# Optimization experiments

Measured on AMD Instinct MI355X. Metric: run time of the kernel, lower is better.

## Reference

```python
import jax, jax.numpy as jnp
import numpy as np

B, L, D, H = 2, 512, 1024, 16
DH = D // H  # head_dim = 64


def setup_inputs() -> dict:
    key = jax.random.key(0)
    ks = jax.random.split(key, 14)
    s = 0.02
    inp = {
        "x": jax.random.normal(ks[0], (B, L, D), jnp.float32),
        "q1_w": jax.random.normal(ks[1], (D, D), jnp.float32) * s,
        "q1_b": jax.random.normal(ks[2], (D,), jnp.float32) * s,
        "k1_w": jax.random.normal(ks[3], (D, D), jnp.float32) * s,
        "k1_b": jax.random.normal(ks[4], (D,), jnp.float32) * s,
        "k2_w": jax.random.normal(ks[5], (D, D), jnp.float32) * s,
        "k2_b": jax.random.normal(ks[6], (D,), jnp.float32) * s,
        "gw_w": jax.random.normal(ks[7], (DH, 1), jnp.float32) * s,
        "gw_b": jax.random.normal(ks[8], (1,), jnp.float32) * s,
        "sw_w": jax.random.normal(ks[9], (DH, 1), jnp.float32) * s,
        "sw_b": jax.random.normal(ks[10], (1,), jnp.float32) * s,
        "cp_w": jax.random.normal(ks[11], (D, D), jnp.float32) * s,
        "cp_b": jax.random.normal(ks[12], (D,), jnp.float32) * s,
    }
    return inp


def reference(x, q1_w, q1_b, k1_w, k1_b, k2_w, k2_b, gw_w, gw_b, sw_w, sw_b, cp_w, cp_b):
    b, l, dm = x.shape
    dh = gw_w.shape[0]
    h = dm // dh
    Q = (x @ q1_w + q1_b).reshape(b, l, h, dh)              # (B,L,H,d)
    K = (x @ k1_w + k1_b).reshape(b, l, h, dh)              # (B,L,H,d)
    V = x.reshape(b, l, h, dh)                               # (B,L,H,d)
    # outer-product state K ⊗ V : (B,L,H,d,d)
    W = K[..., :, None] * V[..., None, :]
    # gate -> stable cumulative product along L (log-space, clamped)
    G = jax.nn.sigmoid(x.reshape(b, l, h, dh) @ gw_w + gw_b)          # (B,L,H,1)
    log_cp = jnp.clip(jnp.cumsum(jnp.log(jnp.clip(G, 1e-6, None)), axis=1), -30.0, 30.0)
    Gc = (jnp.exp(log_cp) + 1e-6)[..., None]                 # (B,L,H,1,1)
    # decay branch
    R = jax.nn.silu(K @ sw_w + sw_b)[..., None]              # (B,L,H,1,1)
    # weighted (invertible) cumsum: cumsum(x / cumprod) * cumprod
    Wc = jnp.cumsum(W * R / Gc, axis=1) * Gc                 # (B,L,H,d,d)
    O1 = jnp.einsum('blhd,blhde->blhe', Q, Wc)               # (B,L,H,d)
    # MA branch on residuals
    E = V[:, 1:] - O1[:, :-1]                                # (B,L-1,H,d)
    sd = jnp.sqrt(jnp.asarray(dh, x.dtype))
    q2 = -jax.nn.leaky_relu(-Q[:, :-1] / sd, 0.02)           # ma_q_activation
    sD = jnp.sqrt(jnp.asarray(dm, x.dtype))
    k2 = jax.nn.sigmoid((x[:, :-1] @ k2_w + k2_b) / sD * 0.02).reshape(b, l - 1, h, dh)
    Wma = jnp.cumsum(k2[..., :, None] * E[..., None, :], axis=1)  # (B,L-1,H,d,d)
    O2 = jnp.einsum('blhd,blhde->blhe', q2, Wma)             # (B,L-1,H,d)
    O2 = jnp.concatenate([jnp.zeros_like(O2[:, :1]), O2], axis=1)  # (B,L,H,d)
    y = (O1 + O2).reshape(b, l, dm)
    return y @ cp_w + cp_b
```

## Files before the change

### kernel.cpp

```cpp
#include <hip/hip_runtime.h>
#include <hip/hip_bf16.h>
#include <math.h>


typedef unsigned short ushort_t;
typedef __attribute__((ext_vector_type(8))) short bf16x8;
typedef __attribute__((ext_vector_type(4))) float f32x4;

__device__ __forceinline__ float sigmoidf_(float z) { return 1.f / (1.f + expf(-z)); }

__device__ __forceinline__ ushort_t f2bf(float f) {
    __hip_bfloat16 h = __float2bfloat16(f);
    return *reinterpret_cast<ushort_t*>(&h);
}

__device__ __forceinline__ float bf2f(ushort_t u) {
    union { unsigned int i; float f; } v;
    v.i = ((unsigned int)u) << 16;
    return v.f;
}

__device__ __forceinline__ void gl16(const void* g, void* l) {
    __builtin_amdgcn_global_load_lds(
        (const __attribute__((address_space(1))) unsigned int*)g,
        (__attribute__((address_space(3))) unsigned int*)l, 16, 0, 0);
}

__global__ __launch_bounds__(256) void cvtT(const float* __restrict__ xs,
                                            const float* __restrict__ w0, const float* __restrict__ w1,
                                            const float* __restrict__ w2, const float* __restrict__ w3,
                                            ushort_t* __restrict__ xd,
                                            ushort_t* __restrict__ t0, ushort_t* __restrict__ t1,
                                            ushort_t* __restrict__ t2, ushort_t* __restrict__ t3) {
    const int blk = blockIdx.x;
    const int tid = threadIdx.x;
    if (blk >= 1024) {
        const int off = ((blk - 1024) * 256 + tid) * 8;
        float4 a = *reinterpret_cast<const float4*>(xs + off);
        float4 b = *reinterpret_cast<const float4*>(xs + off + 4);
        union { uint4 v; ushort_t u[8]; } pk;
        pk.u[0] = f2bf(a.x); pk.u[1] = f2bf(a.y); pk.u[2] = f2bf(a.z); pk.u[3] = f2bf(a.w);
        pk.u[4] = f2bf(b.x); pk.u[5] = f2bf(b.y); pk.u[6] = f2bf(b.z); pk.u[7] = f2bf(b.w);
        *reinterpret_cast<uint4*>(xd + off) = pk.v;
        return;
    }
    const int wi = blk >> 8;
    const float* W = wi == 0 ? w0 : wi == 1 ? w1 : wi == 2 ? w2 : w3;
    ushort_t* WT = wi == 0 ? t0 : wi == 1 ? t1 : wi == 2 ? t2 : t3;
    const int tile = blk & 255;
    const int k0 = (tile >> 4) * 64, n0 = (tile & 15) * 64;
    __shared__ ushort_t T[64][72];
#pragma unroll
    for (int it = 0; it < 4; ++it) {
        const int idx = tid + it * 256;
        const int r = idx >> 4;
        const int c4 = (idx & 15) * 4;
        float4 v = *reinterpret_cast<const float4*>(W + (size_t)(k0 + r) * 1024 + n0 + c4);
        T[r][c4 + 0] = f2bf(v.x); T[r][c4 + 1] = f2bf(v.y);
        T[r][c4 + 2] = f2bf(v.z); T[r][c4 + 3] = f2bf(v.w);
    }
    __syncthreads();
    const int n = tid >> 2;
    const int kq = (tid & 3) * 16;
    union { uint4 v[2]; ushort_t u[16]; } pk;
#pragma unroll
    for (int j = 0; j < 16; ++j) pk.u[j] = T[kq + j][n];
    *reinterpret_cast<uint4*>(WT + (size_t)(n0 + n) * 1024 + k0 + kq) = pk.v[0];
    *reinterpret_cast<uint4*>(WT + (size_t)(n0 + n) * 1024 + k0 + kq + 8) = pk.v[1];
}

__global__ __launch_bounds__(256) void gemmQKC(const ushort_t* __restrict__ Ab,
                                               const ushort_t* __restrict__ WqT,
                                               const ushort_t* __restrict__ WkT,
                                               const ushort_t* __restrict__ WcT,
                                               const float* __restrict__ bq_,
                                               const float* __restrict__ bk_,
                                               const float* __restrict__ bc_,
                                               const float* __restrict__ x,
                                               const float* __restrict__ gww,
                                               const float* __restrict__ gwb,
                                               const float* __restrict__ sww,
                                               const float* __restrict__ swb,
                                               ushort_t* __restrict__ qb,
                                               ushort_t* __restrict__ q2b,
                                               ushort_t* __restrict__ kb,
                                               ushort_t* __restrict__ k2q,
                                               float* __restrict__ gc_out,
                                               float* __restrict__ ab_out,
                                               float* __restrict__ dS0) {
    const int sel = blockIdx.z;
    const ushort_t* WT = sel == 0 ? WqT : sel == 1 ? WkT : WcT;
    const float* bias = sel == 0 ? bq_ : sel == 1 ? bk_ : bc_;
    const int m0 = blockIdx.y * 64, n0 = blockIdx.x * 64;

    __shared__ __align__(16) char smem[32768];

    const int tid = threadIdx.x;
    const int w = tid >> 6, lane = tid & 63;
    const int l15 = lane & 15, lq = lane >> 4;

    f32x4 acc[4];
#pragma unroll
    for (int i = 0; i < 4; ++i) acc[i] = (f32x4){0.f, 0.f, 0.f, 0.f};

    auto stage = [&](int buf, int k0) {
        char* As = smem + buf * 8192;
        char* Bs = smem + 16384 + buf * 8192;
#pragma unroll
        for (int is = 0; is < 2; ++is) {
            const int p = tid * 16 + is * 4096;
            const int row = p >> 7;
            const int scb = (p & 127) ^ ((row & 7) << 4);
            gl16((const char*)Ab + (((size_t)(m0 + row)) << 11) + (k0 << 1) + scb,
                 As + is * 4096 + w * 1024);
            gl16((const char*)WT + (((size_t)(n0 + row)) << 11) + (k0 << 1) + scb,
                 Bs + is * 4096 + w * 1024);
        }
    };

    stage(0, 0);
    __syncthreads();
    for (int k0 = 0; k0 < 1024; k0 += 64) {
        const int cur = (k0 >> 6) & 1;
        if (k0 < 960) stage(cur ^ 1, k0 + 64);
        const char* As = smem + cur * 8192;
        const char* Bs = smem + 16384 + cur * 8192;
#pragma unroll
        for (int kk = 0; kk < 64; kk += 32) {
            const int cb = (kk + 8 * lq) * 2;
            const int ra = 16 * w + l15;
            bf16x8 a = *reinterpret_cast<const bf16x8*>(As + ra * 128 + (cb ^ ((ra & 7) << 4)));
#pragma unroll
            for (int nt = 0; nt < 4; ++nt) {
                const int rb = 16 * nt + l15;
                bf16x8 b = *reinterpret_cast<const bf16x8*>(Bs + rb * 128 + (cb ^ ((rb & 7) << 4)));
                acc[nt] = __builtin_amdgcn_mfma_f32_16x16x32_bf16(a, b, acc[nt], 0, 0, 0);
            }
        }
        __syncthreads();
    }

#pragma unroll
    for (int nt = 0; nt < 4; ++nt) {
        const int col = n0 + 16 * nt + l15;
        const float bcol = bias[col];
#pragma unroll
        for (int r = 0; r < 4; ++r) {
            acc[nt][r] += bcol;
            const int row = m0 + 16 * w + 4 * lq + r;
            const size_t o = (size_t)row * 1024 + col;
            const float v = acc[nt][r];
            if (sel == 0) {
                qb[o] = f2bf(v);
                q2b[o] = f2bf((v < 0.f ? v : 0.02f * v) * 0.125f);
            } else if (sel == 1) {
                kb[o] = f2bf(v);
            } else {
                k2q[o] = f2bf(sigmoidf_(v * 6.25e-4f));
            }
        }
    }

    if (sel != 1) return;

    typedef ushort_t row72[72];
    row72* KT = (row72*)smem;
    row72* VT = (row72*)(smem + 9216);
    float* gwl  = (float*)(smem + 18432);
    float* ctot = (float*)(smem + 18688);
    float* abl  = (float*)(smem + 18720);
    float* dkl  = (float*)(smem + 18976);
    const int b = blockIdx.y >> 3, j = blockIdx.y & 7;
    const int h = blockIdx.x;
    const int bh = b * 16 + h;
    const size_t xbase = (size_t)(b * 512) * 1024 + h * 64;

    if (tid < 64) gwl[tid] = gww[tid];

    {
        const float s0 = sww[l15], s1 = sww[16 + l15], s2 = sww[32 + l15], s3 = sww[48 + l15];
#pragma unroll
        for (int r = 0; r < 4; ++r) {
            float p = acc[0][r] * s0 + acc[1][r] * s1 + acc[2][r] * s2 + acc[3][r] * s3;
            p += __shfl_xor(p, 1, 64);
            p += __shfl_xor(p, 2, 64);
            p += __shfl_xor(p, 4, 64);
            p += __shfl_xor(p, 8, 64);
            if (l15 == 0) dkl[16 * w + 4 * lq + r] = p;
        }
    }
    __syncthreads();

    const float gwbv = gwb[0], swbv = swb[0];
    float ps_own = 0.f;
    for (int i = 0; i * 256 < (j + 1) * 64; ++i) {
        const int t = i * 256 + tid;
        const int cseg = i * 4 + w;
        if (cseg <= j) {
            const float* xr = x + xbase + (size_t)t * 1024;
            float dg = 0.f;
#pragma unroll
            for (int d = 0; d < 64; d += 4) {
                float4 xv = *reinterpret_cast<const float4*>(xr + d);
                dg += xv.x * gwl[d] + xv.y * gwl[d + 1] + xv.z * gwl[d + 2] + xv.w * gwl[d + 3];
            }
            const float g = sigmoidf_(dg + gwbv);
            float ps = logf(fmaxf(g, 1e-6f));
#pragma unroll
            for (int off = 1; off < 64; off <<= 1) {
                float v = __shfl_up(ps, off, 64);
                if (lane >= off) ps += v;
            }
            if (lane == 63) ctot[cseg] = ps;
            if (cseg == j) ps_own = ps;
        }
    }
    __syncthreads();
    if (w == (j & 3)) {
        float coff = 0.f;
        for (int cc = 0; cc < j; ++cc) coff += ctot[cc];
        const float lsum = coff + ps_own;
        const float Gc = expf(fminf(fmaxf(lsum, -30.f), 30.f)) + 1e-6f;
        const float z = dkl[lane] + swbv;
        const float a = z * sigmoidf_(z) / Gc;
        abl[lane] = a;
        gc_out[bh * 512 + j * 64 + lane] = Gc;
        ab_out[bh * 512 + j * 64 + lane] = a;
    }
    __syncthreads();

#pragma unroll
    for (int nt = 0; nt < 4; ++nt)
#pragma unroll
        for (int r = 0; r < 4; ++r)
            KT[16 * nt + l15][16 * w + 4 * lq + r] = f2bf(acc[nt][r]);
#pragma unroll
    for (int it = 0; it < 4; ++it) {
        const int idx = tid + it * 256;
        const int rr = idx >> 4;
        const int c4 = (idx & 15) << 2;
        float4 xv = *reinterpret_cast<const float4*>(x + xbase + (size_t)(j * 64 + rr) * 1024 + c4);
        const float a = abl[rr];
        VT[c4 + 0][rr] = f2bf(a * xv.x); VT[c4 + 1][rr] = f2bf(a * xv.y);
        VT[c4 + 2][rr] = f2bf(a * xv.z); VT[c4 + 3][rr] = f2bf(a * xv.w);
    }
    __syncthreads();

    f32x4 st[4];
#pragma unroll
    for (int n = 0; n < 4; ++n) st[n] = (f32x4){0.f, 0.f, 0.f, 0.f};
#pragma unroll
    for (int kk = 0; kk < 64; kk += 32) {
        bf16x8 ak = *reinterpret_cast<const bf16x8*>(&KT[16 * w + l15][kk + 8 * lq]);
#pragma unroll
        for (int n = 0; n < 4; ++n) {
            bf16x8 vb = *reinterpret_cast<const bf16x8*>(&VT[16 * n + l15][kk + 8 * lq]);
            st[n] = __builtin_amdgcn_mfma_f32_16x16x32_bf16(ak, vb, st[n], 0, 0, 0);
        }
    }
    float* o = dS0 + (size_t)(bh * 8 + j) * 4096;
#pragma unroll
    for (int n = 0; n < 4; ++n)
#pragma unroll
        for (int r = 0; r < 4; ++r)
            o[(16 * w + 4 * lq + r) * 64 + 16 * n + l15] = st[n][r];
}

__global__ __launch_bounds__(512) void out0_ds1(const float* __restrict__ x,
                                                const ushort_t* __restrict__ Qb,
                                                const ushort_t* __restrict__ Kb,
                                                const ushort_t* __restrict__ K2b,
                                                const float* __restrict__ gc,
                                                const float* __restrict__ ab,
                                                const float* __restrict__ dS0,
                                                float* __restrict__ O1out,
                                                float* __restrict__ dS1,
                                                ushort_t* __restrict__ EbT) {
    const int rt = blockIdx.x, bh = blockIdx.y;
    const int b = bh >> 4, h = bh & 15;
    const int c0 = rt * 64;
    const int tid = threadIdx.x;
    const int w = tid >> 6, lane = tid & 63;
    const int l15 = lane & 15, lq = lane >> 4;
    const int tw = w >> 1, eh = w & 1;

    __shared__ __align__(16) char Qs[8192];
    __shared__ __align__(16) char Ks[8192];
    __shared__ ushort_t VT[64][72];
    __shared__ ushort_t K2T[64][72];
    __shared__ ushort_t ET[64][72];
    __shared__ ushort_t Ps[64][72];
    __shared__ ushort_t SBt[64][72];
    __shared__ float av[64], gcv[64];

    const size_t base = (size_t)(b * 512) * 1024 + h * 64;
    const size_t rowB = (size_t)(b * 512 + c0) * 2048 + h * 128;

    {
        const int p = tid * 16;
        const int row = p >> 7;
        const int scb = (p & 127) ^ ((row & 7) << 4);
        gl16((const char*)Qb + rowB + (size_t)row * 2048 + scb, Qs + w * 1024);
        gl16((const char*)Kb + rowB + (size_t)row * 2048 + scb, Ks + w * 1024);
    }
#pragma unroll
    for (int it = 0; it < 2; ++it) {
        const int idx = tid + it * 512;
        const int rr = idx >> 4;
        const int c4 = (idx & 15) << 2;
        const int tau = c0 + rr;
        float4 xv = *reinterpret_cast<const float4*>(x + base + (size_t)tau * 1024 + c4);
        VT[c4 + 0][rr] = f2bf(xv.x); VT[c4 + 1][rr] = f2bf(xv.y);
        VT[c4 + 2][rr] = f2bf(xv.z); VT[c4 + 3][rr] = f2bf(xv.w);
        ushort4 cv = *reinterpret_cast<const ushort4*>(K2b + base + (size_t)tau * 1024 + c4);
        K2T[c4 + 0][rr] = cv.x; K2T[c4 + 1][rr] = cv.y;
        K2T[c4 + 2][rr] = cv.z; K2T[c4 + 3][rr] = cv.w;
    }
    if (tid < 64) av[tid] = ab[bh * 512 + c0 + tid];
    else if (tid < 128) gcv[tid - 64] = gc[bh * 512 + c0 + tid - 64];

#pragma unroll
    for (int ii = 0; ii < 2; ++ii) {
        const int flat = tid * 8 + ii * 4;
        float4 s = {0.f, 0.f, 0.f, 0.f};
        for (int jj = 0; jj < rt; ++jj) {
            float4 v = *reinterpret_cast<const float4*>(dS0 + (size_t)(bh * 8 + jj) * 4096 + flat);
            s.x += v.x; s.y += v.y; s.z += v.z; s.w += v.w;
        }
        const int d = flat >> 6, e = flat & 63;
        SBt[e + 0][d] = f2bf(s.x); SBt[e + 1][d] = f2bf(s.y);
        SBt[e + 2][d] = f2bf(s.z); SBt[e + 3][d] = f2bf(s.w);
    }
    __syncthreads();

    const int ra = 16 * tw + l15;
    f32x4 sc[2];
    sc[0] = (f32x4){0.f, 0.f, 0.f, 0.f};
    sc[1] = (f32x4){0.f, 0.f, 0.f, 0.f};
#pragma unroll
    for (int kk = 0; kk < 64; kk += 32) {
        const int cb = (kk + 8 * lq) * 2;
        bf16x8 aq = *reinterpret_cast<const bf16x8*>(Qs + ra * 128 + (cb ^ ((ra & 7) << 4)));
#pragma unroll
        for (int i = 0; i < 2; ++i) {
            const int rb = 16 * (2 * eh + i) + l15;
            bf16x8 bb = *reinterpret_cast<const bf16x8*>(Ks + rb * 128 + (cb ^ ((rb & 7) << 4)));
            sc[i] = __builtin_amdgcn_mfma_f32_16x16x32_bf16(aq, bb, sc[i], 0, 0, 0);
        }
    }
#pragma unroll
    for (int i = 0; i < 2; ++i) {
        const int cl = 16 * (2 * eh + i) + l15;
#pragma unroll
        for (int r = 0; r < 4; ++r) {
            const int tl = 16 * tw + 4 * lq + r;
            Ps[tl][cl] = f2bf(cl <= tl ? sc[i][r] * av[cl] : 0.f);
        }
    }
    __syncthreads();

    f32x4 oc[2];
    oc[0] = (f32x4){0.f, 0.f, 0.f, 0.f};
    oc[1] = (f32x4){0.f, 0.f, 0.f, 0.f};
#pragma unroll
    for (int kk = 0; kk < 64; kk += 32) {
        const int cb = (kk + 8 * lq) * 2;
        bf16x8 aq = *reinterpret_cast<const bf16x8*>(Qs + ra * 128 + (cb ^ ((ra & 7) << 4)));
        bf16x8 ap = *reinterpret_cast<const bf16x8*>(&Ps[16 * tw + l15][kk + 8 * lq]);
#pragma unroll
        for (int i = 0; i < 2; ++i) {
            const int nb = 16 * (2 * eh + i) + l15;
            bf16x8 sb = *reinterpret_cast<const bf16x8*>(&SBt[nb][kk + 8 * lq]);
            oc[i] = __builtin_amdgcn_mfma_f32_16x16x32_bf16(aq, sb, oc[i], 0, 0, 0);
            bf16x8 vb = *reinterpret_cast<const bf16x8*>(&VT[nb][kk + 8 * lq]);
            oc[i] = __builtin_amdgcn_mfma_f32_16x16x32_bf16(ap, vb, oc[i], 0, 0, 0);
        }
    }

#pragma unroll
    for (int i = 0; i < 2; ++i) {
        const int e = 16 * (2 * eh + i) + l15;
#pragma unroll
        for (int r = 0; r < 4; ++r) {
            const int tl = 16 * tw + 4 * lq + r;
            const int tau = c0 + tl;
            const float val = gcv[tl] * oc[i][r];
            O1out[base + (size_t)tau * 1024 + e] = val;
            float ev = 0.f;
            if (tau <= 510) ev = x[base + (size_t)(tau + 1) * 1024 + e] - val;
            ET[e][tl] = f2bf(ev);
        }
    }
    __syncthreads();

    {
        const int e = tid >> 3;
        const int tq = (tid & 7) * 8;
        uint4 v0 = *reinterpret_cast<const uint4*>(&ET[e][tq]);
        *reinterpret_cast<uint4*>(EbT + (size_t)(bh * 64 + e) * 512 + c0 + tq) = v0;
    }

    f32x4 st[2];
    st[0] = (f32x4){0.f, 0.f, 0.f, 0.f};
    st[1] = (f32x4){0.f, 0.f, 0.f, 0.f};
#pragma unroll
    for (int kk = 0; kk < 64; kk += 32) {
        bf16x8 ak = *reinterpret_cast<const bf16x8*>(&K2T[16 * tw + l15][kk + 8 * lq]);
#pragma unroll
        for (int i = 0; i < 2; ++i) {
            bf16x8 eb = *reinterpret_cast<const bf16x8*>(&ET[16 * (2 * eh + i) + l15][kk + 8 * lq]);
            st[i] = __builtin_amdgcn_mfma_f32_16x16x32_bf16(ak, eb, st[i], 0, 0, 0);
        }
    }
    float* o = dS1 + (size_t)(bh * 8 + rt) * 4096;
#pragma unroll
    for (int i = 0; i < 2; ++i)
#pragma unroll
        for (int r = 0; r < 4; ++r)
            o[(16 * tw + 4 * lq + r) * 64 + 16 * (2 * eh + i) + l15] = st[i][r];
}

__global__ __launch_bounds__(512) void out1_k(const ushort_t* __restrict__ Q2b,
                                              const ushort_t* __restrict__ K2b,
                                              const ushort_t* __restrict__ EbT,
                                              const float* __restrict__ O1,
                                              const float* __restrict__ dS1,
                                              ushort_t* __restrict__ yout) {
    const int rt = blockIdx.x, bh = blockIdx.y;
    const int b = bh >> 4, h = bh & 15;
    const int c0 = rt * 64;
    const int tid = threadIdx.x;
    const int w = tid >> 6, lane = tid & 63;
    const int l15 = lane & 15, lq = lane >> 4;
    const int tw = w >> 1, eh = w & 1;

    __shared__ __align__(16) char Q2s[8192];
    __shared__ __align__(16) char K2s[8192];
    __shared__ __align__(16) char ETs[8192];
    __shared__ ushort_t Ps[64][72];
    __shared__ ushort_t SBt[64][72];

    const size_t base = (size_t)(b * 512) * 1024 + h * 64;
    const size_t rowB = (size_t)(b * 512 + c0) * 2048 + h * 128;

    {
        const int p = tid * 16;
        const int row = p >> 7;
        const int scb = (p & 127) ^ ((row & 7) << 4);
        gl16((const char*)Q2b + rowB + (size_t)row * 2048 + scb, Q2s + w * 1024);
        gl16((const char*)K2b + rowB + (size_t)row * 2048 + scb, K2s + w * 1024);
        gl16((const char*)EbT + (size_t)(bh * 64 + row) * 1024 + c0 * 2 + scb, ETs + w * 1024);
    }
#pragma unroll
    for (int ii = 0; ii < 2; ++ii) {
        const int flat = tid * 8 + ii * 4;
        float4 s = {0.f, 0.f, 0.f, 0.f};
        for (int jj = 0; jj < rt; ++jj) {
            float4 v = *reinterpret_cast<const float4*>(dS1 + (size_t)(bh * 8 + jj) * 4096 + flat);
            s.x += v.x; s.y += v.y; s.z += v.z; s.w += v.w;
        }
        const int d = flat >> 6, e = flat & 63;
        SBt[e + 0][d] = f2bf(s.x); SBt[e + 1][d] = f2bf(s.y);
        SBt[e + 2][d] = f2bf(s.z); SBt[e + 3][d] = f2bf(s.w);
    }
    __syncthreads();

    const int ra = 16 * tw + l15;
    f32x4 sc[2];
    sc[0] = (f32x4){0.f, 0.f, 0.f, 0.f};
    sc[1] = (f32x4){0.f, 0.f, 0.f, 0.f};
#pragma unroll
    for (int kk = 0; kk < 64; kk += 32) {
        const int cb = (kk + 8 * lq) * 2;
        bf16x8 aq = *reinterpret_cast<const bf16x8*>(Q2s + ra * 128 + (cb ^ ((ra & 7) << 4)));
#pragma unroll
        for (int i = 0; i < 2; ++i) {
            const int rb = 16 * (2 * eh + i) + l15;
            bf16x8 bb = *reinterpret_cast<const bf16x8*>(K2s + rb * 128 + (cb ^ ((rb & 7) << 4)));
            sc[i] = __builtin_amdgcn_mfma_f32_16x16x32_bf16(aq, bb, sc[i], 0, 0, 0);
        }
    }
#pragma unroll
    for (int i = 0; i < 2; ++i) {
        const int cl = 16 * (2 * eh + i) + l15;
#pragma unroll
        for (int r = 0; r < 4; ++r) {
            const int tl = 16 * tw + 4 * lq + r;
            Ps[tl][cl] = f2bf(cl <= tl ? sc[i][r] : 0.f);
        }
    }
    __syncthreads();

    f32x4 oc[2];
    oc[0] = (f32x4){0.f, 0.f, 0.f, 0.f};
    oc[1] = (f32x4){0.f, 0.f, 0.f, 0.f};
#pragma unroll
    for (int kk = 0; kk < 64; kk += 32) {
        const int cb = (kk + 8 * lq) * 2;
        bf16x8 aq = *reinterpret_cast<const bf16x8*>(Q2s + ra * 128 + (cb ^ ((ra & 7) << 4)));
        bf16x8 ap = *reinterpret_cast<const bf16x8*>(&Ps[16 * tw + l15][kk + 8 * lq]);
#pragma unroll
        for (int i = 0; i < 2; ++i) {
            const int rb = 16 * (2 * eh + i) + l15;
            bf16x8 sb = *reinterpret_cast<const bf16x8*>(&SBt[rb][kk + 8 * lq]);
            oc[i] = __builtin_amdgcn_mfma_f32_16x16x32_bf16(aq, sb, oc[i], 0, 0, 0);
            bf16x8 eb = *reinterpret_cast<const bf16x8*>(ETs + rb * 128 + (cb ^ ((rb & 7) << 4)));
            oc[i] = __builtin_amdgcn_mfma_f32_16x16x32_bf16(ap, eb, oc[i], 0, 0, 0);
        }
    }

#pragma unroll
    for (int i = 0; i < 2; ++i) {
        const int e = 16 * (2 * eh + i) + l15;
#pragma unroll
        for (int r = 0; r < 4; ++r) {
            const int tp = c0 + 16 * tw + 4 * lq + r;
            if (tp <= 510) {
                yout[(size_t)(b * 512 + tp + 1) * 1024 + h * 64 + e] =
                    f2bf(O1[base + (size_t)(tp + 1) * 1024 + e] + oc[i][r]);
            }
        }
    }
    if (rt == 0 && tid < 64)
        yout[(size_t)(b * 512) * 1024 + h * 64 + tid] = f2bf(O1[base + tid]);
}

__global__ __launch_bounds__(512) void gemmP(const ushort_t* __restrict__ Ab,
                                             const ushort_t* __restrict__ WT,
                                             const float* __restrict__ bias,
                                             float* __restrict__ Out) {
    const int m0 = blockIdx.y * 64, n0 = blockIdx.x * 64;
    __shared__ __align__(16) char smem[32768];

    const int tid = threadIdx.x;
    const int w = tid >> 6, lane = tid & 63;
    const int l15 = lane & 15, lq = lane >> 4;
    const int mw = w >> 1, nh = w & 1;

    f32x4 acc[2];
    acc[0] = (f32x4){0.f, 0.f, 0.f, 0.f};
    acc[1] = (f32x4){0.f, 0.f, 0.f, 0.f};

    auto stage = [&](int buf, int k0) {
        const int p = tid * 16;
        const int row = p >> 7;
        const int scb = (p & 127) ^ ((row & 7) << 4);
        gl16((const char*)Ab + (((size_t)(m0 + row)) << 11) + (k0 << 1) + scb,
             smem + buf * 8192 + w * 1024);
        gl16((const char*)WT + (((size_t)(n0 + row)) << 11) + (k0 << 1) + scb,
             smem + 16384 + buf * 8192 + w * 1024);
    };

    stage(0, 0);
    __syncthreads();
    for (int k0 = 0; k0 < 1024; k0 += 64) {
        const int cur = (k0 >> 6) & 1;
        if (k0 < 960) stage(cur ^ 1, k0 + 64);
        const char* As = smem + cur * 8192;
        const char* Bs = smem + 16384 + cur * 8192;
#pragma unroll
        for (int kk = 0; kk < 64; kk += 32) {
            const int cb = (kk + 8 * lq) * 2;
            const int ra = 16 * mw + l15;
            bf16x8 a = *reinterpret_cast<const bf16x8*>(As + ra * 128 + (cb ^ ((ra & 7) << 4)));
#pragma unroll
            for (int i = 0; i < 2; ++i) {
                const int rb = 16 * (2 * nh + i) + l15;
                bf16x8 b = *reinterpret_cast<const bf16x8*>(Bs + rb * 128 + (cb ^ ((rb & 7) << 4)));
                acc[i] = __builtin_amdgcn_mfma_f32_16x16x32_bf16(a, b, acc[i], 0, 0, 0);
            }
        }
        __syncthreads();
    }
#pragma unroll
    for (int i = 0; i < 2; ++i) {
        const int col = n0 + 16 * (2 * nh + i) + l15;
        const float bcol = bias[col];
#pragma unroll
        for (int r = 0; r < 4; ++r) {
            const int row = m0 + 16 * mw + 4 * lq + r;
            Out[(size_t)row * 1024 + col] = acc[i][r] + bcol;
        }
    }
}

extern "C" void kernel_launch(void* const* d_in, const int* in_sizes, int n_in,
                              void* d_out, int out_size, void* d_ws, size_t ws_size,
                              hipStream_t stream) {
    const float* x   = (const float*)d_in[0];
    const float* q1w = (const float*)d_in[1];
    const float* q1b = (const float*)d_in[2];
    const float* k1w = (const float*)d_in[3];
    const float* k1b = (const float*)d_in[4];
    const float* k2w = (const float*)d_in[5];
    const float* k2b = (const float*)d_in[6];
    const float* gww = (const float*)d_in[7];
    const float* gwb = (const float*)d_in[8];
    const float* sww = (const float*)d_in[9];
    const float* swb = (const float*)d_in[10];
    const float* cpw = (const float*)d_in[11];
    const float* cpb = (const float*)d_in[12];
    float* out = (float*)d_out;

    float* ws = (float*)d_ws;
    float* O1   = ws;
    float* dS0b = ws + 1048576;
    float* dS1b = ws + 2097152;
    float* gcb  = ws + 3145728;
    float* abb  = ws + 3162112;
    ushort_t* ub = (ushort_t*)(ws + 3178496);
    ushort_t* xb   = ub;
    ushort_t* qb   = ub + 1048576;
    ushort_t* q2b  = ub + 2097152;
    ushort_t* kb   = ub + 3145728;
    ushort_t* k2q  = ub + 4194304;
    ushort_t* EbT  = ub + 5242880;
    ushort_t* wqT  = ub + 6291456;
    ushort_t* wkT  = ub + 7340032;
    ushort_t* wcT  = ub + 8388608;
    ushort_t* wpT  = ub + 9437184;
    ushort_t* ytb  = ub + 10485760;

    cvtT<<<1536, 256, 0, stream>>>(x, q1w, k1w, k2w, cpw, xb, wqT, wkT, wcT, wpT);
    gemmQKC<<<dim3(16, 16, 3), 256, 0, stream>>>(xb, wqT, wkT, wcT, q1b, k1b, k2b,
                                                 x, gww, gwb, sww, swb,
                                                 qb, q2b, kb, k2q, gcb, abb, dS0b);
    out0_ds1<<<dim3(8, 32), 512, 0, stream>>>(x, qb, kb, k2q, gcb, abb, dS0b, O1, dS1b, EbT);
    out1_k<<<dim3(8, 32), 512, 0, stream>>>(q2b, k2q, EbT, O1, dS1b, ytb);
    gemmP<<<dim3(16, 16), 512, 0, stream>>>(ytb, wpT, cpb, out);
}
```

Measured before the change: 60.86 us.

## Triple-buffer GEMM LDS staging with explicit vmcnt waits in projection kernels

Both bf16 MFMA GEMM kernels move from double to triple buffering of the A/B tiles in LDS. Loads are issued two iterations ahead, and the full __syncthreads is replaced by partial s_waitcnt vmcnt counts plus raw s_barrier, so global-to-LDS copies can overlap more compute. The loop is fully unrolled. LDS use per block grows from 32KB to 48KB, which may lower occupancy, and the hand-set vmcnt values must match the number of outstanding loads exactly.

Result: faster. 57.52 us (-5.5%).

```diff
diff --git a/kernel.cpp b/kernel.cpp
--- a/kernel.cpp
+++ b/kernel.cpp
@@ -93,7 +93,7 @@
     const float* bias = sel == 0 ? bq_ : sel == 1 ? bk_ : bc_;
     const int m0 = blockIdx.y * 64, n0 = blockIdx.x * 64;
 
-    __shared__ __align__(16) char smem[32768];
+    __shared__ __align__(16) char smem[49152];
 
     const int tid = threadIdx.x;
     const int w = tid >> 6, lane = tid & 63;
@@ -105,7 +105,7 @@
 
     auto stage = [&](int buf, int k0) {
         char* As = smem + buf * 8192;
-        char* Bs = smem + 16384 + buf * 8192;
+        char* Bs = smem + 24576 + buf * 8192;
 #pragma unroll
         for (int is = 0; is < 2; ++is) {
             const int p = tid * 16 + is * 4096;
@@ -119,12 +119,19 @@
     };
 
     stage(0, 0);
-    __syncthreads();
-    for (int k0 = 0; k0 < 1024; k0 += 64) {
-        const int cur = (k0 >> 6) & 1;
-        if (k0 < 960) stage(cur ^ 1, k0 + 64);
+    stage(1, 64);
+#pragma unroll
+    for (int it = 0; it < 16; ++it) {
+        const int k0 = it * 64;
+        const int cur = it % 3;
+        if (it < 14) stage((it + 2) % 3, k0 + 128);
+        if (it < 14)      asm volatile("s_waitcnt vmcnt(8)" ::: "memory");
+        else if (it == 14) asm volatile("s_waitcnt vmcnt(4)" ::: "memory");
+        else               asm volatile("s_waitcnt vmcnt(0)" ::: "memory");
+        __builtin_amdgcn_sched_barrier(0);
+        __builtin_amdgcn_s_barrier();
         const char* As = smem + cur * 8192;
-        const char* Bs = smem + 16384 + cur * 8192;
+        const char* Bs = smem + 24576 + cur * 8192;
 #pragma unroll
         for (int kk = 0; kk < 64; kk += 32) {
             const int cb = (kk + 8 * lq) * 2;
@@ -137,7 +144,9 @@
                 acc[nt] = __builtin_amdgcn_mfma_f32_16x16x32_bf16(a, b, acc[nt], 0, 0, 0);
             }
         }
-        __syncthreads();
+        asm volatile("s_waitcnt lgkmcnt(0)" ::: "memory");
+        __builtin_amdgcn_sched_barrier(0);
+        __builtin_amdgcn_s_barrier();
     }
 
 #pragma unroll
@@ -530,7 +539,7 @@
                                              const float* __restrict__ bias,
                                              float* __restrict__ Out) {
     const int m0 = blockIdx.y * 64, n0 = blockIdx.x * 64;
-    __shared__ __align__(16) char smem[32768];
+    __shared__ __align__(16) char smem[49152];
 
     const int tid = threadIdx.x;
     const int w = tid >> 6, lane = tid & 63;
@@ -548,16 +557,23 @@
         gl16((const char*)Ab + (((size_t)(m0 + row)) << 11) + (k0 << 1) + scb,
              smem + buf * 8192 + w * 1024);
         gl16((const char*)WT + (((size_t)(n0 + row)) << 11) + (k0 << 1) + scb,
-             smem + 16384 + buf * 8192 + w * 1024);
+             smem + 24576 + buf * 8192 + w * 1024);
     };
 
     stage(0, 0);
-    __syncthreads();
-    for (int k0 = 0; k0 < 1024; k0 += 64) {
-        const int cur = (k0 >> 6) & 1;
-        if (k0 < 960) stage(cur ^ 1, k0 + 64);
+    stage(1, 64);
+#pragma unroll
+    for (int it = 0; it < 16; ++it) {
+        const int k0 = it * 64;
+        const int cur = it % 3;
+        if (it < 14) stage((it + 2) % 3, k0 + 128);
+        if (it < 14)      asm volatile("s_waitcnt vmcnt(4)" ::: "memory");
+        else if (it == 14) asm volatile("s_waitcnt vmcnt(2)" ::: "memory");
+        else               asm volatile("s_waitcnt vmcnt(0)" ::: "memory");
+        __builtin_amdgcn_sched_barrier(0);
+        __builtin_amdgcn_s_barrier();
         const char* As = smem + cur * 8192;
-        const char* Bs = smem + 16384 + cur * 8192;
+        const char* Bs = smem + 24576 + cur * 8192;
 #pragma unroll
         for (int kk = 0; kk < 64; kk += 32) {
             const int cb = (kk + 8 * lq) * 2;
@@ -570,7 +586,9 @@
                 acc[i] = __builtin_amdgcn_mfma_f32_16x16x32_bf16(a, b, acc[i], 0, 0, 0);
             }
         }
-        __syncthreads();
+        asm volatile("s_waitcnt lgkmcnt(0)" ::: "memory");
+        __builtin_amdgcn_sched_barrier(0);
+        __builtin_amdgcn_s_barrier();
     }
 #pragma unroll
     for (int i = 0; i < 2; ++i) {
```
